# Performance work log

Measured on AMD Instinct MI355X. Metric: run time of the kernel, lower is better.

Reference implementation:

```python
import jax, jax.numpy as jnp
from jax import lax
import numpy as np

B, L, IN_DIM = 1, 2048, 1024
D_MODEL, D_INNER, D_STATE, DT_RANK, D_CONV, N_LAYERS = 512, 1024, 16, 32, 4, 2


def _ln(x, w, b):
    m = jnp.mean(x, -1, keepdims=True)
    v = jnp.var(x, -1, keepdims=True)
    return (x - m) * lax.rsqrt(v + 1e-5) * w + b


def _rms(x, w):
    return x * lax.rsqrt(jnp.mean(x * x, -1, keepdims=True) + 1e-5) * w


def _assoc_scan(dA, dBx):
    # first-order linear recurrence h_t = dA_t * h_{t-1} + dBx_t via associative scan
    def comb(e1, e2):
        a1, b1 = e1
        a2, b2 = e2
        return a1 * a2, a2 * b1 + b2
    return lax.associative_scan(comb, (dA, dBx), axis=1)[1]


def _mamba_layer(h, in_w, cw, cb, xw, dtw, dtb, alog, Dp, ow, rw):
    hn = _rms(h, rw)                              # pre-norm (RMSNorm)
    xz = hn @ in_w                                # [b,l,2*d_inner]
    xi, z = jnp.split(xz, 2, -1)
    # causal depthwise conv1d (kernel d_conv, left pad d_conv-1)
    xc = lax.conv_general_dilated(xi.transpose(0, 2, 1), cw, (1,), [(D_CONV - 1, 0)],
                                  feature_group_count=D_INNER,
                                  dimension_numbers=('NCH', 'OIH', 'NCH')) + cb[None, :, None]
    xi = jax.nn.silu(xc.transpose(0, 2, 1))       # [b,l,d_inner]
    dbc = xi @ xw                                 # [b,l,dt_rank+2*d_state]
    dt, Bm, Cm = jnp.split(dbc, [DT_RANK, DT_RANK + D_STATE], -1)
    delta = jax.nn.softplus(dt @ dtw + dtb)       # [b,l,d_inner]
    A = -jnp.exp(alog)                            # [d_inner, d_state]
    dA = jnp.exp(delta[..., None] * A)            # [b,l,d_inner,d_state]
    dBx = (delta * xi)[..., None] * Bm[:, :, None, :]
    hs = _assoc_scan(dA, dBx)                     # [b,l,d_inner,d_state]
    y = jnp.einsum('bldn,bln->bld', hs, Cm) + xi * Dp
    y = y * jax.nn.silu(z)
    return h + y @ ow


def _conv_t(x, w, b, s, p):
    # PyTorch ConvTranspose2d, weight layout [Cin, Cout, k, k]
    kT = jnp.flip(w, (2, 3)).transpose(1, 0, 2, 3)
    pad = w.shape[2] - 1 - p
    y = lax.conv_general_dilated(x, kT, (1, 1), [(pad, pad), (pad, pad)],
                                 lhs_dilation=(s, s),
                                 dimension_numbers=('NCHW', 'OIHW', 'NCHW'))
    return y + b[None, :, None, None]


def _fwd(x, coords, W_fc1, b_fc1, W_pos, b_pos,
         mamba_in_w, mamba_conv_w, mamba_conv_b, mamba_x_w, mamba_dt_w, mamba_dt_b,
         mamba_A_log, mamba_D, mamba_out_w, mamba_rms_w,
         ln_w, ln_b, Wa1, ba1, Wa2, ba2,
         ct1_w, ct1_b, ct2_w, ct2_b, ct3_w, ct3_b, ct4_w, ct4_b, ct5_w, ct5_b):
    h = jax.nn.gelu(x @ W_fc1 + b_fc1, approximate=False)   # _fc1
    h = h + (coords @ W_pos + b_pos)[None]                  # linear pos-emb
    for l in range(N_LAYERS):
        h = _mamba_layer(h, mamba_in_w[l], mamba_conv_w[l], mamba_conv_b[l],
                         mamba_x_w[l], mamba_dt_w[l], mamba_dt_b[l],
                         mamba_A_log[l], mamba_D[l], mamba_out_w[l], mamba_rms_w[l])
    h = _ln(h, ln_w, ln_b)
    A = jnp.tanh(h @ Wa1 + ba1) @ Wa2 + ba2                 # [1,L,1]
    A = jax.nn.softmax(A.transpose(0, 2, 1), axis=-1)       # [1,1,L]
    pooled = jnp.einsum('bol,bld->bod', A, h)               # [1,1,512]
    feat = pooled.reshape(x.shape[0], D_MODEL, 1, 1)
    y = jax.nn.relu(_conv_t(feat, ct1_w, ct1_b, 1, 0))      # 1 -> 4
    y = jax.nn.relu(_conv_t(y, ct2_w, ct2_b, 4, 0))         # 4 -> 16
    y = jax.nn.relu(_conv_t(y, ct3_w, ct3_b, 2, 1))         # 16 -> 32
    y = jax.nn.relu(_conv_t(y, ct4_w, ct4_b, 2, 1))         # 32 -> 64
    return _conv_t(y, ct5_w, ct5_b, 2, 1)                   # 64 -> 128, 11 classes


def setup_inputs() -> dict:
    key = jax.random.key(0)
    ks = jax.random.split(key, 32)
    n = lambda k, s, sc=0.02: jax.random.normal(k, s, jnp.float32) * sc
    inp = {
        'x': jax.random.normal(ks[0], (B, L, IN_DIM), jnp.float32),
        'coords': jax.random.uniform(ks[1], (L, 2), jnp.float32),
        'W_fc1': n(ks[2], (IN_DIM, D_MODEL)), 'b_fc1': jnp.zeros((D_MODEL,)),
        'W_pos': n(ks[3], (2, D_MODEL)), 'b_pos': jnp.zeros((D_MODEL,)),
        'mamba_in_w': n(ks[4], (N_LAYERS, D_MODEL, 2 * D_INNER)),
        'mamba_conv_w': n(ks[5], (N_LAYERS, D_INNER, 1, D_CONV), 0.1),
        'mamba_conv_b': jnp.zeros((N_LAYERS, D_INNER)),
        'mamba_x_w': n(ks[6], (N_LAYERS, D_INNER, DT_RANK + 2 * D_STATE)),
        'mamba_dt_w': n(ks[7], (N_LAYERS, DT_RANK, D_INNER), 0.1),
        'mamba_dt_b': jnp.full((N_LAYERS, D_INNER), -4.0, jnp.float32),
        'mamba_A_log': jnp.tile(jnp.log(jnp.arange(1, D_STATE + 1, dtype=jnp.float32)), (N_LAYERS, D_INNER, 1)),
        'mamba_D': jnp.ones((N_LAYERS, D_INNER), jnp.float32),
        'mamba_out_w': n(ks[8], (N_LAYERS, D_INNER, D_MODEL)),
        'mamba_rms_w': jnp.ones((N_LAYERS, D_MODEL), jnp.float32),
        'ln_w': jnp.ones((D_MODEL,)), 'ln_b': jnp.zeros((D_MODEL,)),
        'Wa1': n(ks[9], (D_MODEL, 128)), 'ba1': jnp.zeros((128,)),
        'Wa2': n(ks[10], (128, 1)), 'ba2': jnp.zeros((1,)),
        'ct1_w': n(ks[11], (512, 256, 4, 4)), 'ct1_b': jnp.zeros((256,)),
        'ct2_w': n(ks[12], (256, 128, 4, 4)), 'ct2_b': jnp.zeros((128,)),
        'ct3_w': n(ks[13], (128, 64, 4, 4)), 'ct3_b': jnp.zeros((64,)),
        'ct4_w': n(ks[14], (64, 32, 4, 4)), 'ct4_b': jnp.zeros((32,)),
        'ct5_w': n(ks[15], (32, 11, 4, 4)), 'ct5_b': jnp.zeros((11,)),
    }
    return inp


def reference(x, coords, W_fc1, b_fc1, W_pos, b_pos,
              mamba_in_w, mamba_conv_w, mamba_conv_b, mamba_x_w, mamba_dt_w, mamba_dt_b,
              mamba_A_log, mamba_D, mamba_out_w, mamba_rms_w,
              ln_w, ln_b, Wa1, ba1, Wa2, ba2,
              ct1_w, ct1_b, ct2_w, ct2_b, ct3_w, ct3_b, ct4_w, ct4_b, ct5_w, ct5_b):
    return _fwd(x, coords, W_fc1, b_fc1, W_pos, b_pos,
                mamba_in_w, mamba_conv_w, mamba_conv_b, mamba_x_w, mamba_dt_w, mamba_dt_b,
                mamba_A_log, mamba_D, mamba_out_w, mamba_rms_w,
                ln_w, ln_b, Wa1, ba1, Wa2, ba2,
                ct1_w, ct1_b, ct2_w, ct2_b, ct3_w, ct3_b, ct4_w, ct4_b, ct5_w, ct5_b)
```

## Files before the change

### kernel.cpp

```cpp
#include <hip/hip_runtime.h>
#include <math.h>

#define LSEQ 2048
#define DM 512
#define DI 1024
#define NST 16
#define CHUNK 128
#define NC (LSEQ / CHUNK)

__device__ __forceinline__ float siluf(float v) { return v / (1.f + expf(-v)); }

__global__ __launch_bounds__(256) void gemm64(
    const float* __restrict__ A, int lda,
    const float* __restrict__ B, int ldb,
    float* __restrict__ C, int ldc,
    int K, int accum)
{
    __shared__ float As[16][68];
    __shared__ float Bs[16][68];
    const int tid = threadIdx.x;
    const int tx = tid & 15, ty = tid >> 4;
    const int m0 = blockIdx.y << 6, n0 = blockIdx.x << 6;
    const int arow = tid >> 2, akk = (tid & 3) << 2;
    const int bkr = tid >> 4, bnn = (tid & 15) << 2;
    const float* Ap = A + (size_t)(m0 + arow) * lda + akk;
    const float* Bp = B + (size_t)bkr * ldb + n0 + bnn;
    float acc[4][4] = {};
    for (int k0 = 0; k0 < K; k0 += 16) {
        float4 av = *(const float4*)(Ap + k0);
        float4 bv = *(const float4*)(Bp + (size_t)k0 * ldb);
        As[akk + 0][arow] = av.x;
        As[akk + 1][arow] = av.y;
        As[akk + 2][arow] = av.z;
        As[akk + 3][arow] = av.w;
        *(float4*)&Bs[bkr][bnn] = bv;
        __syncthreads();
#pragma unroll
        for (int kk = 0; kk < 16; ++kk) {
            float4 a = *(const float4*)&As[kk][ty << 2];
            float4 b = *(const float4*)&Bs[kk][tx << 2];
            acc[0][0] = fmaf(a.x, b.x, acc[0][0]);
            acc[0][1] = fmaf(a.x, b.y, acc[0][1]);
            acc[0][2] = fmaf(a.x, b.z, acc[0][2]);
            acc[0][3] = fmaf(a.x, b.w, acc[0][3]);
            acc[1][0] = fmaf(a.y, b.x, acc[1][0]);
            acc[1][1] = fmaf(a.y, b.y, acc[1][1]);
            acc[1][2] = fmaf(a.y, b.z, acc[1][2]);
            acc[1][3] = fmaf(a.y, b.w, acc[1][3]);
            acc[2][0] = fmaf(a.z, b.x, acc[2][0]);
            acc[2][1] = fmaf(a.z, b.y, acc[2][1]);
            acc[2][2] = fmaf(a.z, b.z, acc[2][2]);
            acc[2][3] = fmaf(a.z, b.w, acc[2][3]);
            acc[3][0] = fmaf(a.w, b.x, acc[3][0]);
            acc[3][1] = fmaf(a.w, b.y, acc[3][1]);
            acc[3][2] = fmaf(a.w, b.z, acc[3][2]);
            acc[3][3] = fmaf(a.w, b.w, acc[3][3]);
        }
        __syncthreads();
    }
#pragma unroll
    for (int i = 0; i < 4; ++i) {
        float* Cp = C + (size_t)(m0 + (ty << 2) + i) * ldc + n0 + (tx << 2);
        if (accum) {
            Cp[0] += acc[i][0]; Cp[1] += acc[i][1]; Cp[2] += acc[i][2]; Cp[3] += acc[i][3];
        } else {
            Cp[0] = acc[i][0]; Cp[1] = acc[i][1]; Cp[2] = acc[i][2]; Cp[3] = acc[i][3];
        }
    }
}

__global__ __launch_bounds__(256) void gemm128(
    const float* __restrict__ A, int lda,
    const float* __restrict__ B, int ldb,
    float* __restrict__ C, int ldc,
    int K, int accum)
{
    __shared__ float As[8][128];
    __shared__ float Bs[8][128];
    const int tid = threadIdx.x;
    const int tx = tid & 15, ty = tid >> 4;
    const int m0 = blockIdx.y << 7, n0 = blockIdx.x << 7;
    const int arow = tid >> 1, ak = (tid & 1) << 2;
    const int bkr = tid >> 5, bcol = (tid & 31) << 2;
    const float* Ap = A + (size_t)(m0 + arow) * lda + ak;
    const float* Bp = B + (size_t)bkr * ldb + n0 + bcol;
    float acc[8][8] = {};
    for (int k0 = 0; k0 < K; k0 += 8) {
        float4 av = *(const float4*)(Ap + k0);
        float4 bv = *(const float4*)(Bp + (size_t)k0 * ldb);
        As[ak + 0][arow] = av.x;
        As[ak + 1][arow] = av.y;
        As[ak + 2][arow] = av.z;
        As[ak + 3][arow] = av.w;
        *(float4*)&Bs[bkr][bcol] = bv;
        __syncthreads();
#pragma unroll
        for (int kk = 0; kk < 8; ++kk) {
            float4 a0 = *(const float4*)&As[kk][ty << 2];
            float4 a1 = *(const float4*)&As[kk][(ty << 2) + 64];
            float4 b0 = *(const float4*)&Bs[kk][tx << 2];
            float4 b1 = *(const float4*)&Bs[kk][(tx << 2) + 64];
            float a[8] = {a0.x, a0.y, a0.z, a0.w, a1.x, a1.y, a1.z, a1.w};
            float b[8] = {b0.x, b0.y, b0.z, b0.w, b1.x, b1.y, b1.z, b1.w};
#pragma unroll
            for (int i = 0; i < 8; ++i)
#pragma unroll
                for (int j = 0; j < 8; ++j)
                    acc[i][j] = fmaf(a[i], b[j], acc[i][j]);
        }
        __syncthreads();
    }
#pragma unroll
    for (int qi = 0; qi < 2; ++qi)
#pragma unroll
        for (int i = 0; i < 4; ++i) {
            const int row = m0 + (ty << 2) + i + (qi << 6);
            float* Cp = C + (size_t)row * ldc + n0 + (tx << 2);
            if (accum) {
#pragma unroll
                for (int j = 0; j < 4; ++j) {
                    Cp[j] += acc[(qi << 2) + i][j];
                    Cp[64 + j] += acc[(qi << 2) + i][4 + j];
                }
            } else {
#pragma unroll
                for (int j = 0; j < 4; ++j) {
                    Cp[j] = acc[(qi << 2) + i][j];
                    Cp[64 + j] = acc[(qi << 2) + i][4 + j];
                }
            }
        }
}

__global__ __launch_bounds__(256) void xproj_splitk(
    const float* __restrict__ A, const float* __restrict__ B,
    float* __restrict__ part)
{
    __shared__ float As[16][68];
    __shared__ float Bs[16][68];
    const int tid = threadIdx.x;
    const int tx = tid & 15, ty = tid >> 4;
    const int ks = blockIdx.x;
    const int m0 = blockIdx.y << 6;
    const int arow = tid >> 2, ak = (tid & 3) << 2;
    const int bkr = tid >> 4, bcol = (tid & 15) << 2;
    const int kbase = ks << 7;
    const float* Ap = A + (size_t)(m0 + arow) * DI + kbase + ak;
    const float* Bp = B + (size_t)(kbase + bkr) * 64 + bcol;
    float acc[4][4] = {};
    for (int k0 = 0; k0 < 128; k0 += 16) {
        float4 av = *(const float4*)(Ap + k0);
        float4 bv = *(const float4*)(Bp + k0 * 64);
        As[ak + 0][arow] = av.x;
        As[ak + 1][arow] = av.y;
        As[ak + 2][arow] = av.z;
        As[ak + 3][arow] = av.w;
        *(float4*)&Bs[bkr][bcol] = bv;
        __syncthreads();
#pragma unroll
        for (int kk = 0; kk < 16; ++kk) {
            float4 a = *(const float4*)&As[kk][ty << 2];
            float4 b = *(const float4*)&Bs[kk][tx << 2];
            acc[0][0] = fmaf(a.x, b.x, acc[0][0]);
            acc[0][1] = fmaf(a.x, b.y, acc[0][1]);
            acc[0][2] = fmaf(a.x, b.z, acc[0][2]);
            acc[0][3] = fmaf(a.x, b.w, acc[0][3]);
            acc[1][0] = fmaf(a.y, b.x, acc[1][0]);
            acc[1][1] = fmaf(a.y, b.y, acc[1][1]);
            acc[1][2] = fmaf(a.y, b.z, acc[1][2]);
            acc[1][3] = fmaf(a.y, b.w, acc[1][3]);
            acc[2][0] = fmaf(a.z, b.x, acc[2][0]);
            acc[2][1] = fmaf(a.z, b.y, acc[2][1]);
            acc[2][2] = fmaf(a.z, b.z, acc[2][2]);
            acc[2][3] = fmaf(a.z, b.w, acc[2][3]);
            acc[3][0] = fmaf(a.w, b.x, acc[3][0]);
            acc[3][1] = fmaf(a.w, b.y, acc[3][1]);
            acc[3][2] = fmaf(a.w, b.z, acc[3][2]);
            acc[3][3] = fmaf(a.w, b.w, acc[3][3]);
        }
        __syncthreads();
    }
#pragma unroll
    for (int i = 0; i < 4; ++i) {
        float* Cp = part + ((size_t)ks * LSEQ + m0 + (ty << 2) + i) * 64 + (tx << 2);
        Cp[0] = acc[i][0]; Cp[1] = acc[i][1]; Cp[2] = acc[i][2]; Cp[3] = acc[i][3];
    }
}

__global__ __launch_bounds__(256) void xproj_reduce(
    const float* __restrict__ part, float* __restrict__ dbc)
{
    const int idx = blockIdx.x * 256 + threadIdx.x;
    float s = 0.f;
#pragma unroll
    for (int ks = 0; ks < 8; ++ks) s += part[(size_t)ks * LSEQ * 64 + idx];
    dbc[idx] = s;
}

__global__ __launch_bounds__(256) void fc1_epi(
    const float* __restrict__ tmp, const float* __restrict__ bfc1,
    const float* __restrict__ coords, const float* __restrict__ Wpos,
    const float* __restrict__ bpos, float* __restrict__ h)
{
    int idx = blockIdx.x * 256 + threadIdx.x;
    int t = idx >> 9, j = idx & 511;
    float v = tmp[idx] + bfc1[j];
    float g = 0.5f * v * (1.f + erff(v * 0.70710678118654752f));
    h[idx] = g + coords[2 * t] * Wpos[j] + coords[2 * t + 1] * Wpos[DM + j] + bpos[j];
}

__global__ __launch_bounds__(256) void rmsnorm_k(
    const float* __restrict__ h, const float* __restrict__ w, float* __restrict__ out)
{
    const int t = blockIdx.x, tid = threadIdx.x;
    float a = h[(size_t)t * DM + tid];
    float b = h[(size_t)t * DM + 256 + tid];
    float ss = a * a + b * b;
#pragma unroll
    for (int off = 1; off < 64; off <<= 1) ss += __shfl_xor(ss, off);
    __shared__ float red[4];
    if ((tid & 63) == 0) red[tid >> 6] = ss;
    __syncthreads();
    float tot = red[0] + red[1] + red[2] + red[3];
    float inv = rsqrtf(tot * (1.f / DM) + 1e-5f);
    out[(size_t)t * DM + tid] = a * inv * w[tid];
    out[(size_t)t * DM + 256 + tid] = b * inv * w[256 + tid];
}

__global__ __launch_bounds__(256) void layernorm_k(
    const float* __restrict__ h, const float* __restrict__ w,
    const float* __restrict__ bb, float* __restrict__ out)
{
    const int t = blockIdx.x, tid = threadIdx.x;
    float a = h[(size_t)t * DM + tid];
    float b = h[(size_t)t * DM + 256 + tid];
    float s = a + b;
#pragma unroll
    for (int off = 1; off < 64; off <<= 1) s += __shfl_xor(s, off);
    __shared__ float red1[4];
    if ((tid & 63) == 0) red1[tid >> 6] = s;
    __syncthreads();
    float mean = (red1[0] + red1[1] + red1[2] + red1[3]) * (1.f / DM);
    float da = a - mean, db = b - mean;
    float vs = da * da + db * db;
#pragma unroll
    for (int off = 1; off < 64; off <<= 1) vs += __shfl_xor(vs, off);
    __shared__ float red2[4];
    if ((tid & 63) == 0) red2[tid >> 6] = vs;
    __syncthreads();
    float var = (red2[0] + red2[1] + red2[2] + red2[3]) * (1.f / DM);
    float inv = rsqrtf(var + 1e-5f);
    out[(size_t)t * DM + tid] = da * inv * w[tid] + bb[tid];
    out[(size_t)t * DM + 256 + tid] = db * inv * w[256 + tid] + bb[256 + tid];
}

__global__ __launch_bounds__(256) void conv_silu_k(
    const float* __restrict__ xz, const float* __restrict__ cw,
    const float* __restrict__ cb, float* __restrict__ xc)
{
    int idx = blockIdx.x * 256 + threadIdx.x;
    int t = idx >> 10, c = idx & 1023;
    float w0 = cw[c * 4], w1 = cw[c * 4 + 1], w2 = cw[c * 4 + 2], w3 = cw[c * 4 + 3];
    float s = cb[c];
    if (t >= 3) s = fmaf(xz[(size_t)(t - 3) * 2048 + c], w0, s);
    if (t >= 2) s = fmaf(xz[(size_t)(t - 2) * 2048 + c], w1, s);
    if (t >= 1) s = fmaf(xz[(size_t)(t - 1) * 2048 + c], w2, s);
    s = fmaf(xz[(size_t)t * 2048 + c], w3, s);
    xc[idx] = siluf(s);
}

__global__ __launch_bounds__(256) void softplus_k(
    float* __restrict__ delta, const float* __restrict__ dtb)
{
    int idx = blockIdx.x * 256 + threadIdx.x;
    int d = idx & 1023;
    float v = delta[idx] + dtb[d];
    delta[idx] = fmaxf(v, 0.f) + log1pf(expf(-fabsf(v)));
}

__global__ __launch_bounds__(256) void scan_p1(
    const float* __restrict__ delta, const float* __restrict__ xc,
    const float* __restrict__ dbc, const float* __restrict__ alog,
    float* __restrict__ aprod, float* __restrict__ hfin)
{
    __shared__ float sD[CHUNK][16], sX[CHUNK][16], sB[CHUNK][16];
    const int tid = threadIdx.x;
    const int g = tid >> 4, n = tid & 15;
    const int d0 = blockIdx.x << 4;
    const int c = blockIdx.y;
    const int t0 = c * CHUNK;
    const int d = d0 + g;
    const float An = -expf(alog[d * NST + n]);
    for (int i = tid; i < CHUNK * 16; i += 256) {
        int r = i >> 4, cc = i & 15;
        sD[r][cc] = delta[(size_t)(t0 + r) * DI + d0 + cc];
        sX[r][cc] = xc[(size_t)(t0 + r) * DI + d0 + cc];
        sB[r][cc] = dbc[(size_t)(t0 + r) * 64 + 32 + cc];
    }
    __syncthreads();
    float h = 0.f, ap = 1.f;
    for (int i = 0; i < CHUNK; ++i) {
        float dl = sD[i][g], xv = sX[i][g];
        float a = expf(dl * An);
        h = fmaf(a, h, dl * xv * sB[i][n]);
        ap *= a;
    }
    size_t idx = ((size_t)c * DI + d) * NST + n;
    aprod[idx] = ap;
    hfin[idx] = h;
}

__global__ __launch_bounds__(256) void scan_carry(
    const float* __restrict__ aprod, const float* __restrict__ hfin,
    float* __restrict__ carry)
{
    const int dn = blockIdx.x * 256 + threadIdx.x;
    float h = 0.f;
    carry[dn] = 0.f;
#pragma unroll
    for (int c = 0; c < NC - 1; ++c) {
        h = fmaf(aprod[(size_t)c * DI * NST + dn], h, hfin[(size_t)c * DI * NST + dn]);
        carry[(size_t)(c + 1) * DI * NST + dn] = h;
    }
}

__global__ __launch_bounds__(256) void scan_p2(
    const float* __restrict__ delta, const float* __restrict__ xc,
    const float* __restrict__ dbc, const float* __restrict__ xz,
    const float* __restrict__ alog, const float* __restrict__ Dp,
    const float* __restrict__ carry, float* __restrict__ y)
{
    __shared__ float sD[CHUNK][16], sX[CHUNK][16], sB[CHUNK][16], sC[CHUNK][16], sZ[CHUNK][16];
    const int tid = threadIdx.x;
    const int g = tid >> 4, n = tid & 15;
    const int d0 = blockIdx.x << 4;
    const int c = blockIdx.y;
    const int t0 = c * CHUNK;
    const int d = d0 + g;
    const float An = -expf(alog[d * NST + n]);
    const float Dd = Dp[d];
    for (int i = tid; i < CHUNK * 16; i += 256) {
        int r = i >> 4, cc = i & 15;
        sD[r][cc] = delta[(size_t)(t0 + r) * DI + d0 + cc];
        sX[r][cc] = xc[(size_t)(t0 + r) * DI + d0 + cc];
        sB[r][cc] = dbc[(size_t)(t0 + r) * 64 + 32 + cc];
        sC[r][cc] = dbc[(size_t)(t0 + r) * 64 + 48 + cc];
        sZ[r][cc] = xz[(size_t)(t0 + r) * 2048 + 1024 + d0 + cc];
    }
    __syncthreads();
    float h = carry[((size_t)c * DI + d) * NST + n];
    for (int i = 0; i < CHUNK; ++i) {
        float dl = sD[i][g], xv = sX[i][g];
        float a = expf(dl * An);
        h = fmaf(a, h, dl * xv * sB[i][n]);
        float p = h * sC[i][n];
        p += __shfl_xor(p, 1, 16);
        p += __shfl_xor(p, 2, 16);
        p += __shfl_xor(p, 4, 16);
        p += __shfl_xor(p, 8, 16);
        if (n == 0) {
            float yv = p + xv * Dd;
            float zz = sZ[i][g];
            y[(size_t)(t0 + i) * DI + d] = yv * siluf(zz);
        }
    }
}

__global__ __launch_bounds__(256) void attn_fin(
    const float* __restrict__ amx, const float* __restrict__ ba1,
    const float* __restrict__ Wa2, const float* __restrict__ ba2,
    float* __restrict__ scores)
{
    const int tid = threadIdx.x;
    const int row = blockIdx.x * 4 + (tid >> 6);
    const int lane = tid & 63;
    float v = tanhf(amx[(size_t)row * 128 + lane] + ba1[lane]) * Wa2[lane]
            + tanhf(amx[(size_t)row * 128 + 64 + lane] + ba1[64 + lane]) * Wa2[64 + lane];
#pragma unroll
    for (int off = 1; off < 64; off <<= 1) v += __shfl_xor(v, off);
    if (lane == 0) scores[row] = v + ba2[0];
}

__global__ __launch_bounds__(1024) void softmax_k(
    const float* __restrict__ s, float* __restrict__ w)
{
    const int tid = threadIdx.x;
    __shared__ float red[16];
    float m = fmaxf(s[tid], s[tid + 1024]);
#pragma unroll
    for (int off = 1; off < 64; off <<= 1) m = fmaxf(m, __shfl_xor(m, off));
    if ((tid & 63) == 0) red[tid >> 6] = m;
    __syncthreads();
    if (tid < 64) {
        float mm = (tid < 16) ? red[tid] : -1e30f;
#pragma unroll
        for (int off = 1; off < 16; off <<= 1) mm = fmaxf(mm, __shfl_xor(mm, off));
        if (tid == 0) red[0] = mm;
    }
    __syncthreads();
    const float gm = red[0];
    __syncthreads();
    float e0 = expf(s[tid] - gm), e1 = expf(s[tid + 1024] - gm);
    float sum = e0 + e1;
#pragma unroll
    for (int off = 1; off < 64; off <<= 1) sum += __shfl_xor(sum, off);
    __shared__ float red2[16];
    if ((tid & 63) == 0) red2[tid >> 6] = sum;
    __syncthreads();
    if (tid < 64) {
        float ss = (tid < 16) ? red2[tid] : 0.f;
#pragma unroll
        for (int off = 1; off < 16; off <<= 1) ss += __shfl_xor(ss, off);
        if (tid == 0) red2[0] = ss;
    }
    __syncthreads();
    float inv = 1.f / red2[0];
    w[tid] = e0 * inv;
    w[tid + 1024] = e1 * inv;
}

__global__ __launch_bounds__(256) void pooled_p1(
    const float* __restrict__ wts, const float* __restrict__ hf, float* __restrict__ part)
{
    const int j = blockIdx.x * 256 + threadIdx.x;
    const int tc = blockIdx.y;
    float acc = 0.f;
    const int t0 = tc * 128;
    for (int t = t0; t < t0 + 128; ++t) acc = fmaf(wts[t], hf[(size_t)t * DM + j], acc);
    part[(size_t)tc * DM + j] = acc;
}

__global__ __launch_bounds__(256) void pooled_p2(
    const float* __restrict__ part, float* __restrict__ pooled)
{
    const int j = blockIdx.x * 256 + threadIdx.x;
    float acc = 0.f;
#pragma unroll
    for (int tc = 0; tc < 16; ++tc) acc += part[(size_t)tc * DM + j];
    pooled[j] = acc;
}

__global__ __launch_bounds__(256) void ct1_fast(
    const float* __restrict__ feat, const float* __restrict__ w,
    const float* __restrict__ b, float* __restrict__ out)
{
    __shared__ float sf[512];
    __shared__ float sRed[256];
    const int o = blockIdx.x, tid = threadIdx.x;
    sf[tid] = feat[tid];
    sf[tid + 256] = feat[tid + 256];
    __syncthreads();
    const int p = tid & 15, g = tid >> 4;
    float acc = 0.f;
#pragma unroll 8
    for (int ci = g * 32; ci < g * 32 + 32; ++ci)
        acc = fmaf(sf[ci], w[ci * 4096 + (o << 4) + p], acc);
    sRed[tid] = acc;
    __syncthreads();
    if (g == 0) {
        float s = b[o];
#pragma unroll
        for (int gg = 0; gg < 16; ++gg) s += sRed[gg * 16 + p];
        out[(o << 4) + p] = fmaxf(s, 0.f);
    }
}

__global__ __launch_bounds__(256) void ct2_fast(
    const float* __restrict__ in, const float* __restrict__ w,
    const float* __restrict__ b, float* __restrict__ out)
{
    __shared__ float sI[1024];
    __shared__ float sW[1024];
    __shared__ float sRed[256];
    const int yy = blockIdx.x, o = blockIdx.y, tid = threadIdx.x;
    const int iy = yy >> 2, ky = yy & 3;
    for (int i = tid; i < 1024; i += 256) {
        int ci = i >> 2, q = i & 3;
        sI[i] = in[(ci << 4) + (iy << 2) + q];
        sW[i] = w[ci * 2048 + (o << 4) + (ky << 2) + q];
    }
    __syncthreads();
    const int xx = tid & 15, g = tid >> 4;
    const int ix = xx >> 2, kx = xx & 3;
    float acc = 0.f;
#pragma unroll 8
    for (int ci = g * 16; ci < g * 16 + 16; ++ci)
        acc = fmaf(sI[(ci << 2) + ix], sW[(ci << 2) + kx], acc);
    sRed[tid] = acc;
    __syncthreads();
    if (g == 0) {
        float s = b[o];
#pragma unroll
        for (int gg = 0; gg < 16; ++gg) s += sRed[gg * 16 + xx];
        out[(o << 8) + (yy << 4) + xx] = fmaxf(s, 0.f);
    }
}

__global__ __launch_bounds__(256) void ctup_fast(
    const float* __restrict__ in, const float* __restrict__ w,
    const float* __restrict__ b, float* __restrict__ out,
    int Cin, int Cout, int Hin, int hshift, int relu)
{
    __shared__ float sIn[4608];
    __shared__ float sW[2048];
    __shared__ float sRed[256];
    const int tid = threadIdx.x;
    const int yy = blockIdx.x, o = blockIdx.y;
    const int Hout = Hin << 1;
    const int ST = Hin + 2;
    const int houtshift = hshift + 1;

    const int ky0 = (yy + 1) & 1;
    const int iy0 = (yy + 1 - ky0) >> 1;
    const int iy1 = iy0 - 1;
    const int row_elems = Cin * ST;

    for (int i = tid; i < 2 * row_elems; i += 256) sIn[i] = 0.f;
    __syncthreads();
    const int nload = Cin << hshift;
    if (iy0 < Hin) {
        const float* src = in + ((size_t)iy0 << hshift);
        for (int i = tid; i < nload; i += 256) {
            int ci = i >> hshift, col = i & (Hin - 1);
            sIn[ci * ST + 1 + col] = src[((size_t)ci << (2 * hshift)) + col];
        }
    }
    if (iy1 >= 0) {
        const float* src = in + ((size_t)iy1 << hshift);
        for (int i = tid; i < nload; i += 256) {
            int ci = i >> hshift, col = i & (Hin - 1);
            sIn[row_elems + ci * ST + 1 + col] = src[((size_t)ci << (2 * hshift)) + col];
        }
    }
    for (int i = tid; i < (Cin << 4); i += 256)
        sW[i] = w[(size_t)(i >> 4) * (Cout << 4) + (o << 4) + (i & 15)];
    __syncthreads();

    const int xx = tid & (Hout - 1);
    const int g = tid >> houtshift;
    const int kx0 = (xx + 1) & 1;
    const int ix0 = (xx + 1 - kx0) >> 1;
    const int k00 = (ky0 << 2) + kx0;

    float acc = 0.f;
    const float* in1 = sIn + row_elems;
#pragma unroll 4
    for (int ci = g * 16; ci < g * 16 + 16; ++ci) {
        const int base = ci * ST + ix0;
        const float* wr = &sW[ci << 4];
        float i00 = sIn[base + 1], i01 = sIn[base];
        float i10 = in1[base + 1], i11 = in1[base];
        acc = fmaf(i00, wr[k00], acc);
        acc = fmaf(i01, wr[k00 + 2], acc);
        acc = fmaf(i10, wr[k00 + 8], acc);
        acc = fmaf(i11, wr[k00 + 10], acc);
    }
    sRed[tid] = acc;
    __syncthreads();
    if (g == 0) {
        float s = b[o];
        const int XG = 256 >> houtshift;
        for (int gg = 0; gg < XG; ++gg) s += sRed[(gg << houtshift) + xx];
        out[(size_t)o * Hout * Hout + (size_t)yy * Hout + xx] = relu ? fmaxf(s, 0.f) : s;
    }
}

extern "C" void kernel_launch(void* const* d_in, const int* in_sizes, int n_in,
                              void* d_out, int out_size, void* d_ws, size_t ws_size,
                              hipStream_t stream)
{
    const float* x      = (const float*)d_in[0];
    const float* coords = (const float*)d_in[1];
    const float* Wfc1   = (const float*)d_in[2];
    const float* bfc1   = (const float*)d_in[3];
    const float* Wpos   = (const float*)d_in[4];
    const float* bpos   = (const float*)d_in[5];
    const float* in_w   = (const float*)d_in[6];
    const float* conv_w = (const float*)d_in[7];
    const float* conv_b = (const float*)d_in[8];
    const float* x_w    = (const float*)d_in[9];
    const float* dt_w   = (const float*)d_in[10];
    const float* dt_b   = (const float*)d_in[11];
    const float* A_log  = (const float*)d_in[12];
    const float* Dp     = (const float*)d_in[13];
    const float* out_w  = (const float*)d_in[14];
    const float* rms_w  = (const float*)d_in[15];
    const float* ln_w   = (const float*)d_in[16];
    const float* ln_b   = (const float*)d_in[17];
    const float* Wa1    = (const float*)d_in[18];
    const float* ba1    = (const float*)d_in[19];
    const float* Wa2    = (const float*)d_in[20];
    const float* ba2    = (const float*)d_in[21];
    const float* ct1w   = (const float*)d_in[22];
    const float* ct1b   = (const float*)d_in[23];
    const float* ct2w   = (const float*)d_in[24];
    const float* ct2b   = (const float*)d_in[25];
    const float* ct3w   = (const float*)d_in[26];
    const float* ct3b   = (const float*)d_in[27];
    const float* ct4w   = (const float*)d_in[28];
    const float* ct4b   = (const float*)d_in[29];
    const float* ct5w   = (const float*)d_in[30];
    const float* ct5b   = (const float*)d_in[31];

    float* ws     = (float*)d_ws;
    float* h      = ws;
    float* hn     = h + (size_t)LSEQ * DM;
    float* xz     = hn + (size_t)LSEQ * DM;
    float* xc     = xz + (size_t)LSEQ * 2 * DI;
    float* dbc    = xc + (size_t)LSEQ * DI;
    float* delta  = dbc + (size_t)LSEQ * 64;
    float* yb     = delta + (size_t)LSEQ * DI;
    float* hf     = yb + (size_t)LSEQ * DI;
    float* scores = hf + (size_t)LSEQ * DM;
    float* wts    = scores + LSEQ;
    float* pooled = wts + LSEQ;
    float* c1     = pooled + DM;
    float* c2     = c1 + 256 * 16;
    float* c3     = c2 + 128 * 256;
    float* c4     = c3 + 64 * 1024;
    float* aprod  = c4 + 32 * 4096;
    float* hfin   = aprod + (size_t)NC * DI * NST;
    float* carry  = hfin + (size_t)NC * DI * NST;
    float* part   = carry + (size_t)NC * DI * NST;
    float* partk  = yb;
    float* amx    = xz;

    gemm64<<<dim3(DM / 64, LSEQ / 64), 256, 0, stream>>>(x, 1024, Wfc1, DM, hn, DM, 1024, 0);
    fc1_epi<<<LSEQ * DM / 256, 256, 0, stream>>>(hn, bfc1, coords, Wpos, bpos, h);

    for (int l = 0; l < 2; ++l) {
        rmsnorm_k<<<LSEQ, 256, 0, stream>>>(h, rms_w + l * DM, hn);
        gemm128<<<dim3(2 * DI / 128, LSEQ / 128), 256, 0, stream>>>(
            hn, DM, in_w + (size_t)l * DM * 2 * DI, 2 * DI, xz, 2 * DI, DM, 0);
        conv_silu_k<<<LSEQ * DI / 256, 256, 0, stream>>>(
            xz, conv_w + (size_t)l * DI * 4, conv_b + (size_t)l * DI, xc);
        xproj_splitk<<<dim3(8, LSEQ / 64), 256, 0, stream>>>(
            xc, x_w + (size_t)l * DI * 64, partk);
        xproj_reduce<<<LSEQ * 64 / 256, 256, 0, stream>>>(partk, dbc);
        gemm64<<<dim3(DI / 64, LSEQ / 64), 256, 0, stream>>>(
            dbc, 64, dt_w + (size_t)l * 32 * DI, DI, delta, DI, 32, 0);
        softplus_k<<<LSEQ * DI / 256, 256, 0, stream>>>(delta, dt_b + (size_t)l * DI);
        scan_p1<<<dim3(DI / 16, NC), 256, 0, stream>>>(
            delta, xc, dbc, A_log + (size_t)l * DI * NST, aprod, hfin);
        scan_carry<<<DI * NST / 256, 256, 0, stream>>>(aprod, hfin, carry);
        scan_p2<<<dim3(DI / 16, NC), 256, 0, stream>>>(
            delta, xc, dbc, xz, A_log + (size_t)l * DI * NST, Dp + (size_t)l * DI,
            carry, yb);
        gemm64<<<dim3(DM / 64, LSEQ / 64), 256, 0, stream>>>(
            yb, DI, out_w + (size_t)l * DI * DM, DM, h, DM, DI, 1);
    }

    layernorm_k<<<LSEQ, 256, 0, stream>>>(h, ln_w, ln_b, hf);
    gemm64<<<dim3(2, LSEQ / 64), 256, 0, stream>>>(hf, DM, Wa1, 128, amx, 128, DM, 0);
    attn_fin<<<LSEQ / 4, 256, 0, stream>>>(amx, ba1, Wa2, ba2, scores);
    softmax_k<<<1, 1024, 0, stream>>>(scores, wts);
    pooled_p1<<<dim3(2, 16), 256, 0, stream>>>(wts, hf, part);
    pooled_p2<<<2, 256, 0, stream>>>(part, pooled);

    ct1_fast<<<256, 256, 0, stream>>>(pooled, ct1w, ct1b, c1);
    ct2_fast<<<dim3(16, 128), 256, 0, stream>>>(c1, ct2w, ct2b, c2);
    ctup_fast<<<dim3(32, 64), 256, 0, stream>>>(c2, ct3w, ct3b, c3, 128, 64, 16, 4, 1);
    ctup_fast<<<dim3(64, 32), 256, 0, stream>>>(c3, ct4w, ct4b, c4, 64, 32, 32, 5, 1);
    ctup_fast<<<dim3(128, 11), 256, 0, stream>>>(c4, ct5w, ct5b, (float*)d_out, 32, 11, 64, 6, 0);
}
```

Baseline: 793.7 us.

## Add register-prefetched 64x128 GEMM with split-K and reduction for projections

New measurement: 670.2 us. 15.6% less time.

```diff
diff --git a/kernel.cpp b/kernel.cpp
--- a/kernel.cpp
+++ b/kernel.cpp
@@ -9,6 +9,74 @@
 #define NC (LSEQ / CHUNK)
 
 __device__ __forceinline__ float siluf(float v) { return v / (1.f + expf(-v)); }
+
+__global__ __launch_bounds__(256) void gemm_mt(
+    const float* __restrict__ A, int lda,
+    const float* __restrict__ B, int ldb,
+    float* __restrict__ out, int ldc, int Ktot)
+{
+    __shared__ float As[16][68];
+    __shared__ float Bs[16][132];
+    const int tid = threadIdx.x;
+    const int tx = tid & 15, ty = tid >> 4;
+    const int n0 = blockIdx.x << 7, m0 = blockIdx.y << 6;
+    const int z = blockIdx.z, nz = gridDim.z;
+    const int Kz = Ktot / nz, kb = z * Kz;
+    const int arow = tid >> 2, ak = (tid & 3) << 2;
+    const int bkr = tid >> 5, bcol = (tid & 31) << 2;
+    const float* Ap = A + (size_t)(m0 + arow) * lda + kb + ak;
+    const float* Bp = B + (size_t)(kb + bkr) * ldb + n0 + bcol;
+    float acc[4][8] = {};
+    float4 av = *(const float4*)(Ap);
+    float4 bv0 = *(const float4*)(Bp);
+    float4 bv1 = *(const float4*)(Bp + (size_t)8 * ldb);
+    for (int k0 = 0; k0 < Kz; k0 += 16) {
+        As[ak + 0][arow] = av.x;
+        As[ak + 1][arow] = av.y;
+        As[ak + 2][arow] = av.z;
+        As[ak + 3][arow] = av.w;
+        *(float4*)&Bs[bkr][bcol] = bv0;
+        *(float4*)&Bs[bkr + 8][bcol] = bv1;
+        __syncthreads();
+        if (k0 + 16 < Kz) {
+            av = *(const float4*)(Ap + k0 + 16);
+            bv0 = *(const float4*)(Bp + (size_t)(k0 + 16) * ldb);
+            bv1 = *(const float4*)(Bp + (size_t)(k0 + 24) * ldb);
+        }
+#pragma unroll
+        for (int kk = 0; kk < 16; ++kk) {
+            float4 a = *(const float4*)&As[kk][ty << 2];
+            float4 b0 = *(const float4*)&Bs[kk][tx << 2];
+            float4 b1 = *(const float4*)&Bs[kk][(tx << 2) + 64];
+            float a4[4] = {a.x, a.y, a.z, a.w};
+            float b8[8] = {b0.x, b0.y, b0.z, b0.w, b1.x, b1.y, b1.z, b1.w};
+#pragma unroll
+            for (int i = 0; i < 4; ++i)
+#pragma unroll
+                for (int j = 0; j < 8; ++j)
+                    acc[i][j] = fmaf(a4[i], b8[j], acc[i][j]);
+        }
+        __syncthreads();
+    }
+    const int Mtot = gridDim.y << 6;
+    float* op = out + (size_t)z * Mtot * ldc;
+#pragma unroll
+    for (int i = 0; i < 4; ++i) {
+        float* Cp = op + (size_t)(m0 + (ty << 2) + i) * ldc + n0 + (tx << 2);
+        *(float4*)Cp = make_float4(acc[i][0], acc[i][1], acc[i][2], acc[i][3]);
+        *(float4*)(Cp + 64) = make_float4(acc[i][4], acc[i][5], acc[i][6], acc[i][7]);
+    }
+}
+
+__global__ __launch_bounds__(256) void sk_reduce(
+    const float* __restrict__ part, float* __restrict__ out, int S, int nz, int add)
+{
+    const int idx = blockIdx.x * 256 + threadIdx.x;
+    if (idx >= S) return;
+    float s = 0.f;
+    for (int zz = 0; zz < nz; ++zz) s += part[(size_t)zz * S + idx];
+    if (add) out[idx] += s; else out[idx] = s;
+}
 
 __global__ __launch_bounds__(256) void gemm64(
     const float* __restrict__ A, int lda,
@@ -67,69 +135,6 @@
             Cp[0] = acc[i][0]; Cp[1] = acc[i][1]; Cp[2] = acc[i][2]; Cp[3] = acc[i][3];
         }
     }
-}
-
-__global__ __launch_bounds__(256) void gemm128(
-    const float* __restrict__ A, int lda,
-    const float* __restrict__ B, int ldb,
-    float* __restrict__ C, int ldc,
-    int K, int accum)
-{
-    __shared__ float As[8][128];
-    __shared__ float Bs[8][128];
-    const int tid = threadIdx.x;
-    const int tx = tid & 15, ty = tid >> 4;
-    const int m0 = blockIdx.y << 7, n0 = blockIdx.x << 7;
-    const int arow = tid >> 1, ak = (tid & 1) << 2;
-    const int bkr = tid >> 5, bcol = (tid & 31) << 2;
-    const float* Ap = A + (size_t)(m0 + arow) * lda + ak;
-    const float* Bp = B + (size_t)bkr * ldb + n0 + bcol;
-    float acc[8][8] = {};
-    for (int k0 = 0; k0 < K; k0 += 8) {
-        float4 av = *(const float4*)(Ap + k0);
-        float4 bv = *(const float4*)(Bp + (size_t)k0 * ldb);
-        As[ak + 0][arow] = av.x;
-        As[ak + 1][arow] = av.y;
-        As[ak + 2][arow] = av.z;
-        As[ak + 3][arow] = av.w;
-        *(float4*)&Bs[bkr][bcol] = bv;
-        __syncthreads();
-#pragma unroll
-        for (int kk = 0; kk < 8; ++kk) {
-            float4 a0 = *(const float4*)&As[kk][ty << 2];
-            float4 a1 = *(const float4*)&As[kk][(ty << 2) + 64];
-            float4 b0 = *(const float4*)&Bs[kk][tx << 2];
-            float4 b1 = *(const float4*)&Bs[kk][(tx << 2) + 64];
-            float a[8] = {a0.x, a0.y, a0.z, a0.w, a1.x, a1.y, a1.z, a1.w};
-            float b[8] = {b0.x, b0.y, b0.z, b0.w, b1.x, b1.y, b1.z, b1.w};
-#pragma unroll
-            for (int i = 0; i < 8; ++i)
-#pragma unroll
-                for (int j = 0; j < 8; ++j)
-                    acc[i][j] = fmaf(a[i], b[j], acc[i][j]);
-        }
-        __syncthreads();
-    }
-#pragma unroll
-    for (int qi = 0; qi < 2; ++qi)
-#pragma unroll
-        for (int i = 0; i < 4; ++i) {
-            const int row = m0 + (ty << 2) + i + (qi << 6);
-            float* Cp = C + (size_t)row * ldc + n0 + (tx << 2);
-            if (accum) {
-#pragma unroll
-                for (int j = 0; j < 4; ++j) {
-                    Cp[j] += acc[(qi << 2) + i][j];
-                    Cp[64 + j] += acc[(qi << 2) + i][4 + j];
-                }
-            } else {
-#pragma unroll
-                for (int j = 0; j < 4; ++j) {
-                    Cp[j] = acc[(qi << 2) + i][j];
-                    Cp[64 + j] = acc[(qi << 2) + i][4 + j];
-                }
-            }
-        }
 }
 
 __global__ __launch_bounds__(256) void xproj_splitk(
@@ -623,15 +628,17 @@
     float* carry  = hfin + (size_t)NC * DI * NST;
     float* part   = carry + (size_t)NC * DI * NST;
     float* partk  = yb;
+    float* skpart = xz;
     float* amx    = xz;
 
-    gemm64<<<dim3(DM / 64, LSEQ / 64), 256, 0, stream>>>(x, 1024, Wfc1, DM, hn, DM, 1024, 0);
+    gemm_mt<<<dim3(DM / 128, LSEQ / 64, 4), 256, 0, stream>>>(x, 1024, Wfc1, DM, skpart, DM, 1024);
+    sk_reduce<<<LSEQ * DM / 256, 256, 0, stream>>>(skpart, hn, LSEQ * DM, 4, 0);
     fc1_epi<<<LSEQ * DM / 256, 256, 0, stream>>>(hn, bfc1, coords, Wpos, bpos, h);
 
     for (int l = 0; l < 2; ++l) {
         rmsnorm_k<<<LSEQ, 256, 0, stream>>>(h, rms_w + l * DM, hn);
-        gemm128<<<dim3(2 * DI / 128, LSEQ / 128), 256, 0, stream>>>(
-            hn, DM, in_w + (size_t)l * DM * 2 * DI, 2 * DI, xz, 2 * DI, DM, 0);
+        gemm_mt<<<dim3(2 * DI / 128, LSEQ / 64, 1), 256, 0, stream>>>(
+            hn, DM, in_w + (size_t)l * DM * 2 * DI, 2 * DI, xz, 2 * DI, DM);
         conv_silu_k<<<LSEQ * DI / 256, 256, 0, stream>>>(
             xz, conv_w + (size_t)l * DI * 4, conv_b + (size_t)l * DI, xc);
         xproj_splitk<<<dim3(8, LSEQ / 64), 256, 0, stream>>>(
@@ -646,8 +653,9 @@
         scan_p2<<<dim3(DI / 16, NC), 256, 0, stream>>>(
             delta, xc, dbc, xz, A_log + (size_t)l * DI * NST, Dp + (size_t)l * DI,
             carry, yb);
-        gemm64<<<dim3(DM / 64, LSEQ / 64), 256, 0, stream>>>(
-            yb, DI, out_w + (size_t)l * DI * DM, DM, h, DM, DI, 1);
+        gemm_mt<<<dim3(DM / 128, LSEQ / 64, 4), 256, 0, stream>>>(
+            yb, DI, out_w + (size_t)l * DI * DM, DM, skpart, DM, 1024);
+        sk_reduce<<<LSEQ * DM / 256, 256, 0, stream>>>(skpart, h, LSEQ * DM, 4, 1);
     }
 
     layernorm_k<<<LSEQ, 256, 0, stream>>>(h, ln_w, ln_b, hf);
```
